# Kernel optimization log

Measured on AMD Instinct MI355X. Metric: run time of the kernel, lower is better.

## Reference

```python
import jax, jax.numpy as jnp
import numpy as np

HUGE = jnp.float32(1e31)   # ops.HUGE_INT
EPS = 1e-20
B, AN = 1024, 256
D = 256            # emb_dim
HD = 512           # history_dim
AD = 2 * D         # action_dim
NE, NR = 100000, 400


def setup_inputs() -> dict:
    key = jax.random.key(0)
    ks = jax.random.split(key, 12)
    e = jax.random.randint(ks[0], (B,), 0, NE)
    q = jax.random.randint(ks[1], (B,), 0, NR)
    hstate = jax.random.normal(ks[2], (B, HD), dtype=jnp.float32)
    r_space = jax.random.randint(ks[3], (B, AN), 0, NR)
    e_space = jax.random.randint(ks[4], (B, AN), 0, NE)
    # binary action mask; guarantee at least one valid action per row
    action_mask = (jax.random.uniform(ks[5], (B, AN)) > 0.2).astype(jnp.float32)
    action_mask = action_mask.at[:, 0].set(1.0)
    entity_emb = jax.random.normal(ks[6], (NE, D), dtype=jnp.float32) * 0.02
    relation_emb = jax.random.normal(ks[7], (NR, D), dtype=jnp.float32) * 0.02
    W1 = jax.random.normal(ks[8], (2 * D + HD, AD), dtype=jnp.float32) * (1.0 / np.sqrt(2 * D + HD))
    b1 = jnp.zeros((AD,), dtype=jnp.float32)
    W2 = jax.random.normal(ks[9], (AD, AD), dtype=jnp.float32) * (1.0 / np.sqrt(AD))
    b2 = jnp.zeros((AD,), dtype=jnp.float32)
    return {"e": e, "q": q, "hstate": hstate, "r_space": r_space,
            "e_space": e_space, "action_mask": action_mask,
            "entity_emb": entity_emb, "relation_emb": relation_emb,
            "W1": W1, "b1": b1, "W2": W2, "b2": b2}


def reference(e, q, hstate, r_space, e_space, action_mask,
              entity_emb, relation_emb, W1, b1, W2, b2):
    Q = relation_emb[q]                       # [B, D]
    E = entity_emb[e]                         # [B, D]
    X = jnp.concatenate([E, hstate, Q], axis=-1)          # [B, 2D+HD]
    X = jax.nn.relu(X @ W1 + b1)                          # [B, AD]
    X2 = X @ W2 + b2                                      # [B, AD]
    # action embeddings: [rel_emb[r]; ent_emb[e]] per padded action slot
    A = jnp.concatenate([relation_emb[r_space], entity_emb[e_space]], axis=-1)  # [B, AN, AD]
    scores = jnp.einsum('bad,bd->ba', A, X2) - (1.0 - action_mask) * HUGE      # [B, AN]
    action_dist = jax.nn.softmax(scores, axis=-1)
    entropy = -jnp.sum(action_dist * jnp.log(jnp.clip(action_dist, EPS)), axis=-1)  # [B]
    return action_dist, entropy
```

## Files before the change

### kernel.cpp

```cpp
#include <hip/hip_runtime.h>
#include <math.h>

#define NB   1024
#define NACT 256
#define DIM  256
#define HDIM 512
#define ADIM 512
#define KTOT 1024
#define NE   100000
#define NR   400
#define NRP  448

typedef __attribute__((ext_vector_type(8))) short bf16x8;
typedef __attribute__((ext_vector_type(4))) float f32x4;

__device__ __forceinline__ unsigned short f2bf(float f) {
    unsigned int u = __float_as_uint(f);
    u += 0x7FFF + ((u >> 16) & 1);
    return (unsigned short)(u >> 16);
}
__device__ __forceinline__ float bf2f(unsigned short u) {
    return __uint_as_float(((unsigned int)u) << 16);
}
__device__ __forceinline__ ushort4 cvt4(float4 v) {
    ushort4 o = {f2bf(v.x), f2bf(v.y), f2bf(v.z), f2bf(v.w)};
    return o;
}

__global__ __launch_bounds__(256) void prep_transpose(
    const float* __restrict__ W1, const float* __restrict__ W2,
    const float* __restrict__ rel,
    ushort* __restrict__ W1T, ushort* __restrict__ W2T,
    ushort* __restrict__ relbf)
{
    const int z = blockIdx.z;
    const int tid = threadIdx.x;
    if (z == 2) {
        const int flat = blockIdx.x * 8 + blockIdx.y;
        const int j = flat * 200 + tid;
        if (tid < 200)
            ((ushort4*)relbf)[j] = cvt4(((const float4*)rel)[j]);
        return;
    }
    __shared__ float t[64][68];
    if (z && blockIdx.x >= 8) return;
    const int Kd = z ? 512 : 1024;
    const float* in = z ? W2 : W1;
    ushort* out = z ? W2T : W1T;
    const int k0 = blockIdx.x * 64, n0 = blockIdx.y * 64;
    const int kr = tid >> 2, c = tid & 3;
    #pragma unroll
    for (int j = 0; j < 4; ++j) {
        const float4 v = *(const float4*)(in + (size_t)(k0 + kr) * ADIM + n0 + c * 16 + j * 4);
        *(float4*)&t[kr][c * 16 + j * 4] = v;
    }
    __syncthreads();
    const int nr = tid >> 2;
    ushort tmp[16];
    #pragma unroll
    for (int kk = 0; kk < 16; ++kk) tmp[kk] = f2bf(t[c * 16 + kk][nr]);
    *(uint4*)(out + (size_t)(n0 + nr) * Kd + k0 + c * 16)     = *(uint4*)&tmp[0];
    *(uint4*)(out + (size_t)(n0 + nr) * Kd + k0 + c * 16 + 8) = *(uint4*)&tmp[8];
}

__global__ __launch_bounds__(256) void gemm1_mfma(
    const float* __restrict__ ent, const float* __restrict__ rel,
    const float* __restrict__ hstate,
    const int* __restrict__ e, const int* __restrict__ q,
    const ushort* __restrict__ W1T, const float* __restrict__ b1,
    ushort* __restrict__ Hbf)
{
    const int tid = threadIdx.x;
    __shared__ __align__(16) ushort Als[64][40];
    __shared__ __align__(16) ushort Bls[64][40];

    const int g  = blockIdx.x;
    const int n0 = (g & 7) * 64;
    const int m0 = (g >> 3) * 64;
    const int wave = tid >> 6, lane = tid & 63;
    const int qq   = lane >> 4, l15 = lane & 15;
    const int sm   = tid >> 2, sc = tid & 3;
    const int kofs = sc * 8;

    const int row   = m0 + sm;
    const float* rowE = ent + (size_t)e[row] * DIM;
    const float* rowH = hstate + (size_t)row * HDIM - DIM;
    const float* rowQ = rel + (size_t)q[row] * DIM - (DIM + HDIM);
    const uint4* gb = (const uint4*)(W1T + (size_t)(n0 + sm) * KTOT) + sc;

    f32x4 acc[4];
    #pragma unroll
    for (int mt = 0; mt < 4; ++mt) acc[mt] = (f32x4){0.f, 0.f, 0.f, 0.f};

    float4 pa0 = *(const float4*)(rowE + kofs);
    float4 pa1 = *(const float4*)(rowE + kofs + 4);
    uint4  pb  = gb[0];

    for (int it = 0; it < KTOT / 32; ++it) {
        ushort t8[8];
        t8[0] = f2bf(pa0.x); t8[1] = f2bf(pa0.y); t8[2] = f2bf(pa0.z); t8[3] = f2bf(pa0.w);
        t8[4] = f2bf(pa1.x); t8[5] = f2bf(pa1.y); t8[6] = f2bf(pa1.z); t8[7] = f2bf(pa1.w);
        *(uint4*)&Als[sm][sc * 8] = *(uint4*)t8;
        *(uint4*)&Bls[sm][sc * 8] = pb;
        __syncthreads();
        if (it + 1 < KTOT / 32) {
            const int kg = (it + 1) * 32 + kofs;
            const float* src = (kg < DIM) ? rowE : ((kg < DIM + HDIM) ? rowH : rowQ);
            pa0 = *(const float4*)(src + kg);
            pa1 = *(const float4*)(src + kg + 4);
            pb  = gb[(it + 1) * 4];
        }
        const bf16x8 bfrag = *(const bf16x8*)&Bls[wave * 16 + l15][qq * 8];
        #pragma unroll
        for (int mt = 0; mt < 4; ++mt) {
            const bf16x8 afrag = *(const bf16x8*)&Als[mt * 16 + l15][qq * 8];
            acc[mt] = __builtin_amdgcn_mfma_f32_16x16x32_bf16(afrag, bfrag, acc[mt], 0, 0, 0);
        }
        __syncthreads();
    }
    const int n = n0 + wave * 16 + l15;
    const float bv = b1[n];
    #pragma unroll
    for (int mt = 0; mt < 4; ++mt)
        #pragma unroll
        for (int r = 0; r < 4; ++r) {
            const int m = m0 + mt * 16 + qq * 4 + r;
            Hbf[(size_t)m * ADIM + n] = f2bf(fmaxf(acc[mt][r] + bv, 0.0f));
        }
}

__global__ __launch_bounds__(256) void gemm2_mfma(
    const ushort* __restrict__ A, const ushort* __restrict__ Bt,
    const float* __restrict__ bias, float* __restrict__ X2up,
    ushort* __restrict__ X2rbf)
{
    __shared__ __align__(16) ushort Als[64][40];
    __shared__ __align__(16) ushort Bls[64][40];
    const int tid  = threadIdx.x;
    const int n0   = blockIdx.x * 64;
    const int m0   = blockIdx.y * 64;
    const int wave = tid >> 6, lane = tid & 63;
    const int qq   = lane >> 4, l15 = lane & 15;
    const int sm   = tid >> 2, sc = tid & 3;

    const uint4* ga = (const uint4*)(A  + (size_t)(m0 + sm) * ADIM) + sc;
    const uint4* gb = (const uint4*)(Bt + (size_t)(n0 + sm) * ADIM) + sc;

    f32x4 acc[4];
    #pragma unroll
    for (int mt = 0; mt < 4; ++mt) acc[mt] = (f32x4){0.f, 0.f, 0.f, 0.f};

    uint4 pa = ga[0], pb = gb[0];
    for (int it = 0; it < ADIM / 32; ++it) {
        *(uint4*)&Als[sm][sc * 8] = pa;
        *(uint4*)&Bls[sm][sc * 8] = pb;
        __syncthreads();
        if (it + 1 < ADIM / 32) {
            pa = ga[(it + 1) * 4];
            pb = gb[(it + 1) * 4];
        }
        const bf16x8 bfrag = *(const bf16x8*)&Bls[wave * 16 + l15][qq * 8];
        #pragma unroll
        for (int mt = 0; mt < 4; ++mt) {
            const bf16x8 afrag = *(const bf16x8*)&Als[mt * 16 + l15][qq * 8];
            acc[mt] = __builtin_amdgcn_mfma_f32_16x16x32_bf16(afrag, bfrag, acc[mt], 0, 0, 0);
        }
        __syncthreads();
    }
    const int n = n0 + wave * 16 + l15;
    const float bv = bias[n];
    #pragma unroll
    for (int mt = 0; mt < 4; ++mt)
        #pragma unroll
        for (int r = 0; r < 4; ++r) {
            const int m = m0 + mt * 16 + qq * 4 + r;
            const float v = acc[mt][r] + bv;
            if (n < 256) X2rbf[(size_t)m * DIM + n] = f2bf(v);
            else         X2up [(size_t)m * DIM + (n - 256)] = v;
        }
}

__global__ __launch_bounds__(256) void gemm_rel(
    const ushort* __restrict__ A, const ushort* __restrict__ Bt,
    float* __restrict__ R)
{
    __shared__ __align__(16) ushort Als[64][40];
    __shared__ __align__(16) ushort Bls[64][40];
    const int tid  = threadIdx.x;
    const int n0   = blockIdx.x * 64;
    const int m0   = blockIdx.y * 64;
    const int wave = tid >> 6, lane = tid & 63;
    const int qq   = lane >> 4, l15 = lane & 15;
    const int sm   = tid >> 2, sc = tid & 3;

    const int brow = (n0 + sm < NR) ? (n0 + sm) : (NR - 1);
    const uint4* ga = (const uint4*)(A  + (size_t)(m0 + sm) * DIM) + sc;
    const uint4* gb = (const uint4*)(Bt + (size_t)brow * DIM) + sc;

    f32x4 acc[4];
    #pragma unroll
    for (int mt = 0; mt < 4; ++mt) acc[mt] = (f32x4){0.f, 0.f, 0.f, 0.f};

    uint4 pa = ga[0], pb = gb[0];
    for (int it = 0; it < DIM / 32; ++it) {
        *(uint4*)&Als[sm][sc * 8] = pa;
        *(uint4*)&Bls[sm][sc * 8] = pb;
        __syncthreads();
        if (it + 1 < DIM / 32) {
            pa = ga[(it + 1) * 4];
            pb = gb[(it + 1) * 4];
        }
        const bf16x8 bfrag = *(const bf16x8*)&Bls[wave * 16 + l15][qq * 8];
        #pragma unroll
        for (int mt = 0; mt < 4; ++mt) {
            const bf16x8 afrag = *(const bf16x8*)&Als[mt * 16 + l15][qq * 8];
            acc[mt] = __builtin_amdgcn_mfma_f32_16x16x32_bf16(afrag, bfrag, acc[mt], 0, 0, 0);
        }
        __syncthreads();
    }
    const int n = n0 + wave * 16 + l15;
    if (n < NR) {
        #pragma unroll
        for (int mt = 0; mt < 4; ++mt)
            #pragma unroll
            for (int r = 0; r < 4; ++r) {
                const int m = m0 + mt * 16 + qq * 4 + r;
                R[(size_t)m * NRP + n] = acc[mt][r];
            }
    }
}

__global__ __launch_bounds__(512) void scores_kernel(
    const int* __restrict__ r_space, const int* __restrict__ e_space,
    const float* __restrict__ amask,
    const float* __restrict__ ent, const float* __restrict__ R,
    const float* __restrict__ X2up,
    float* __restrict__ dist_out, float* __restrict__ ent_out)
{
    const int b    = blockIdx.x;
    const int tid  = threadIdx.x;
    const int wave = tid >> 6;
    const int lane = tid & 63;

    __shared__ float xs[DIM];
    __shared__ float sc[NACT];
    __shared__ int   ridx[NACT];
    __shared__ int   eidx[NACT];
    __shared__ float red1[8], red2[8], red3[8];

    if (tid < NACT) ridx[tid] = r_space[(size_t)b * NACT + tid];
    else            eidx[tid - NACT] = e_space[(size_t)b * NACT + tid - NACT];
    if (tid < DIM / 4)
        ((float4*)xs)[tid] = ((const float4*)(X2up + (size_t)b * DIM))[tid];
    __syncthreads();

    const float4 xe = ((const float4*)xs)[lane];
    const float* R_row = R + (size_t)b * NRP;

    const int abase = wave * 32;
    for (int a0 = abase; a0 < abase + 32; a0 += 16) {
        const float rsc = (lane < 16) ? R_row[ridx[a0 + lane]] : 0.0f;
        float4 ev[16];
        #pragma unroll
        for (int i = 0; i < 16; ++i)
            ev[i] = ((const float4*)(ent + (size_t)eidx[a0 + i] * DIM))[lane];
        float p[16];
        #pragma unroll
        for (int i = 0; i < 16; ++i)
            p[i] = ev[i].x * xe.x + ev[i].y * xe.y + ev[i].z * xe.z + ev[i].w * xe.w;
        #pragma unroll
        for (int off = 32; off; off >>= 1) {
            #pragma unroll
            for (int i = 0; i < 16; ++i) p[i] += __shfl_xor(p[i], off);
        }
        float out = p[0];
        #pragma unroll
        for (int i = 1; i < 16; ++i) out = (lane == i) ? p[i] : out;
        if (lane < 16) sc[a0 + lane] = out + rsc;
    }
    __syncthreads();

    float s = -3.0e38f;
    if (tid < NACT) {
        const float m = amask[(size_t)b * NACT + tid];
        s = sc[tid] - (1.0f - m) * 1e31f;
    }

    float mx = s;
    #pragma unroll
    for (int off = 32; off; off >>= 1) mx = fmaxf(mx, __shfl_xor(mx, off));
    if (lane == 0) red1[wave] = mx;
    __syncthreads();
    mx = red1[0];
    #pragma unroll
    for (int w = 1; w < 8; ++w) mx = fmaxf(mx, red1[w]);

    const float ex = (tid < NACT) ? expf(s - mx) : 0.0f;
    float sum = ex;
    #pragma unroll
    for (int off = 32; off; off >>= 1) sum += __shfl_xor(sum, off);
    if (lane == 0) red2[wave] = sum;
    __syncthreads();
    sum = ((red2[0] + red2[1]) + (red2[2] + red2[3]))
        + ((red2[4] + red2[5]) + (red2[6] + red2[7]));

    const float d = ex / sum;
    if (tid < NACT) dist_out[(size_t)b * NACT + tid] = d;

    float t = (tid < NACT) ? d * logf(fmaxf(d, 1e-20f)) : 0.0f;
    #pragma unroll
    for (int off = 32; off; off >>= 1) t += __shfl_xor(t, off);
    if (lane == 0) red3[wave] = t;
    __syncthreads();
    if (tid == 0)
        ent_out[b] = -(((red3[0] + red3[1]) + (red3[2] + red3[3]))
                     + ((red3[4] + red3[5]) + (red3[6] + red3[7])));
}

extern "C" void kernel_launch(void* const* d_in, const int* in_sizes, int n_in,
                              void* d_out, int out_size, void* d_ws, size_t ws_size,
                              hipStream_t stream) {
    const int*   e       = (const int*)d_in[0];
    const int*   q       = (const int*)d_in[1];
    const float* hstate  = (const float*)d_in[2];
    const int*   r_space = (const int*)d_in[3];
    const int*   e_space = (const int*)d_in[4];
    const float* amask   = (const float*)d_in[5];
    const float* ent     = (const float*)d_in[6];
    const float* rel     = (const float*)d_in[7];
    const float* W1      = (const float*)d_in[8];
    const float* b1      = (const float*)d_in[9];
    const float* W2      = (const float*)d_in[10];
    const float* b2      = (const float*)d_in[11];

    ushort* W1T   = (ushort*)d_ws;
    ushort* W2T   = W1T   + (size_t)ADIM * KTOT;
    ushort* Hbf   = W2T   + (size_t)ADIM * ADIM;
    ushort* relbf = Hbf   + (size_t)NB * ADIM;
    ushort* X2rbf = relbf + (size_t)NR * DIM;
    float*  X2up  = (float*)(X2rbf + (size_t)NB * DIM);
    float*  Rtab  = X2up + (size_t)NB * DIM;
    float*  dist  = (float*)d_out;
    float*  entr  = dist + (size_t)NB * NACT;

    prep_transpose<<<dim3(16, 8, 3), 256, 0, stream>>>(W1, W2, rel, W1T, W2T, relbf);
    gemm1_mfma<<<128, 256, 0, stream>>>(ent, rel, hstate, e, q, W1T, b1, Hbf);
    gemm2_mfma<<<dim3(ADIM / 64, NB / 64), 256, 0, stream>>>(Hbf, W2T, b2, X2up, X2rbf);
    gemm_rel<<<dim3(NRP / 64, NB / 64), 256, 0, stream>>>(X2rbf, relbf, Rtab);
    scores_kernel<<<NB, 512, 0, stream>>>(
        r_space, e_space, amask, ent, Rtab, X2up, dist, entr);
}
```

Before: 228.1 us.

## Fold relation GEMM into W2 via precomputed rel·W2 and split-K GEMMs

Precomputes rel_emb·W2_low (a 400x512 product) so the relation score table comes straight out of the second GEMM, which removes the separate gemm_rel launch and the bf16 X2 round trip. GEMM1 is split-K into four partial buffers to get more blocks, and the reduction, bias and ReLU are fused into the second GEMM's A-operand load. The second GEMM is also split-K by two, so the scores kernel has to add the two partials. In exchange there is more fp32 partial traffic and a different bf16 rounding path for the relation scores.

```diff
diff --git a/kernel.cpp b/kernel.cpp
--- a/kernel.cpp
+++ b/kernel.cpp
@@ -10,6 +10,7 @@
 #define NE   100000
 #define NR   400
 #define NRP  448
+#define NCAT 704
 
 typedef __attribute__((ext_vector_type(8))) short bf16x8;
 typedef __attribute__((ext_vector_type(4))) float f32x4;
@@ -19,95 +20,147 @@
     u += 0x7FFF + ((u >> 16) & 1);
     return (unsigned short)(u >> 16);
 }
-__device__ __forceinline__ float bf2f(unsigned short u) {
-    return __uint_as_float(((unsigned int)u) << 16);
-}
 __device__ __forceinline__ ushort4 cvt4(float4 v) {
     ushort4 o = {f2bf(v.x), f2bf(v.y), f2bf(v.z), f2bf(v.w)};
     return o;
 }
 
-__global__ __launch_bounds__(256) void prep_transpose(
+__global__ __launch_bounds__(256) void prep_kernel(
     const float* __restrict__ W1, const float* __restrict__ W2,
-    const float* __restrict__ rel,
-    ushort* __restrict__ W1T, ushort* __restrict__ W2T,
-    ushort* __restrict__ relbf)
+    const float* __restrict__ rel, const float* __restrict__ b2,
+    ushort* __restrict__ W1T, ushort* __restrict__ Bcat,
+    ushort* __restrict__ W2lowbf, ushort* __restrict__ relbf,
+    float* __restrict__ cvec)
 {
-    const int z = blockIdx.z;
-    const int tid = threadIdx.x;
-    if (z == 2) {
-        const int flat = blockIdx.x * 8 + blockIdx.y;
-        const int j = flat * 200 + tid;
-        if (tid < 200)
-            ((ushort4*)relbf)[j] = cvt4(((const float4*)rel)[j]);
-        return;
-    }
-    __shared__ float t[64][68];
-    if (z && blockIdx.x >= 8) return;
-    const int Kd = z ? 512 : 1024;
-    const float* in = z ? W2 : W1;
-    ushort* out = z ? W2T : W1T;
-    const int k0 = blockIdx.x * 64, n0 = blockIdx.y * 64;
-    const int kr = tid >> 2, c = tid & 3;
-    #pragma unroll
-    for (int j = 0; j < 4; ++j) {
-        const float4 v = *(const float4*)(in + (size_t)(k0 + kr) * ADIM + n0 + c * 16 + j * 4);
-        *(float4*)&t[kr][c * 16 + j * 4] = v;
-    }
-    __syncthreads();
-    const int nr = tid >> 2;
-    ushort tmp[16];
-    #pragma unroll
-    for (int kk = 0; kk < 16; ++kk) tmp[kk] = f2bf(t[c * 16 + kk][nr]);
-    *(uint4*)(out + (size_t)(n0 + nr) * Kd + k0 + c * 16)     = *(uint4*)&tmp[0];
-    *(uint4*)(out + (size_t)(n0 + nr) * Kd + k0 + c * 16 + 8) = *(uint4*)&tmp[8];
-}
-
-__global__ __launch_bounds__(256) void gemm1_mfma(
+    const int blk = blockIdx.x, tid = threadIdx.x;
+    if (blk < 160) {
+        __shared__ float t[64][68];
+        const float* in; ushort* out; int Kd, k0, n0, rowbase;
+        if (blk < 128) {
+            in = W1; out = W1T; Kd = 1024;
+            k0 = (blk >> 3) * 64; n0 = (blk & 7) * 64; rowbase = n0;
+        } else {
+            const int l = blk - 128;
+            in = W2; out = Bcat; Kd = 512;
+            k0 = (l >> 2) * 64; n0 = 256 + (l & 3) * 64; rowbase = n0 - 256;
+        }
+        const int kr = tid >> 2, c = tid & 3;
+        #pragma unroll
+        for (int j = 0; j < 4; ++j) {
+            const float4 v = *(const float4*)(in + (size_t)(k0 + kr) * ADIM + n0 + c * 16 + j * 4);
+            *(float4*)&t[kr][c * 16 + j * 4] = v;
+        }
+        __syncthreads();
+        const int nr = tid >> 2;
+        ushort tmp[16];
+        #pragma unroll
+        for (int kk = 0; kk < 16; ++kk) tmp[kk] = f2bf(t[c * 16 + kk][nr]);
+        *(uint4*)(out + (size_t)(rowbase + nr) * Kd + k0 + c * 16)     = *(uint4*)&tmp[0];
+        *(uint4*)(out + (size_t)(rowbase + nr) * Kd + k0 + c * 16 + 8) = *(uint4*)&tmp[8];
+    } else if (blk < 288) {
+        const int l = blk - 160;
+        const int row = l * 4 + (tid >> 6);
+        const int d4  = tid & 63;
+        const float4 v = *(const float4*)(W2 + (size_t)row * ADIM + d4 * 4);
+        *(ushort4*)(W2lowbf + (size_t)row * DIM + d4 * 4) = cvt4(v);
+    } else if (blk < 388) {
+        const int j = (blk - 288) * 256 + tid;
+        ((ushort4*)relbf)[j] = cvt4(((const float4*)rel)[j]);
+    } else {
+        const int r = (blk - 388) * 256 + tid;
+        if (r < NRP) {
+            const int rr = (r < NR) ? r : (NR - 1);
+            const float* a = rel + (size_t)rr * DIM;
+            float s = 0.f;
+            for (int d = 0; d < DIM; d += 4) {
+                const float4 av = *(const float4*)(a + d);
+                const float4 bv = *(const float4*)(b2 + d);
+                s += av.x * bv.x + av.y * bv.y + av.z * bv.z + av.w * bv.w;
+            }
+            cvec[r] = s;
+        }
+    }
+}
+
+__global__ __launch_bounds__(256) void mega2_kernel(
     const float* __restrict__ ent, const float* __restrict__ rel,
     const float* __restrict__ hstate,
     const int* __restrict__ e, const int* __restrict__ q,
-    const ushort* __restrict__ W1T, const float* __restrict__ b1,
-    ushort* __restrict__ Hbf)
+    const ushort* __restrict__ W1T, const ushort* __restrict__ relbf,
+    const ushort* __restrict__ W2lowbf,
+    ushort* __restrict__ Bcat, float* __restrict__ Hpart)
 {
-    const int tid = threadIdx.x;
     __shared__ __align__(16) ushort Als[64][40];
     __shared__ __align__(16) ushort Bls[64][40];
-
-    const int g  = blockIdx.x;
-    const int n0 = (g & 7) * 64;
-    const int m0 = (g >> 3) * 64;
+    const int blk = blockIdx.x, tid = threadIdx.x;
     const int wave = tid >> 6, lane = tid & 63;
     const int qq   = lane >> 4, l15 = lane & 15;
     const int sm   = tid >> 2, sc = tid & 3;
-    const int kofs = sc * 8;
-
-    const int row   = m0 + sm;
-    const float* rowE = ent + (size_t)e[row] * DIM;
-    const float* rowH = hstate + (size_t)row * HDIM - DIM;
-    const float* rowQ = rel + (size_t)q[row] * DIM - (DIM + HDIM);
-    const uint4* gb = (const uint4*)(W1T + (size_t)(n0 + sm) * KTOT) + sc;
 
     f32x4 acc[4];
     #pragma unroll
     for (int mt = 0; mt < 4; ++mt) acc[mt] = (f32x4){0.f, 0.f, 0.f, 0.f};
 
-    float4 pa0 = *(const float4*)(rowE + kofs);
-    float4 pa1 = *(const float4*)(rowE + kofs + 4);
+    if (blk < 56) {
+        const int n0 = (blk & 7) * 64;
+        const int m0 = (blk >> 3) * 64;
+        const int arow = (m0 + sm < NR) ? (m0 + sm) : (NR - 1);
+        const uint4* ga = (const uint4*)(relbf + (size_t)arow * DIM) + sc;
+        const uint4* gb = (const uint4*)(W2lowbf + (size_t)(n0 + sm) * DIM) + sc;
+        uint4 pa = ga[0], pb = gb[0];
+        for (int it = 0; it < DIM / 32; ++it) {
+            *(uint4*)&Als[sm][sc * 8] = pa;
+            *(uint4*)&Bls[sm][sc * 8] = pb;
+            __syncthreads();
+            if (it + 1 < DIM / 32) { pa = ga[(it + 1) * 4]; pb = gb[(it + 1) * 4]; }
+            const bf16x8 bfrag = *(const bf16x8*)&Bls[wave * 16 + l15][qq * 8];
+            #pragma unroll
+            for (int mt = 0; mt < 4; ++mt) {
+                const bf16x8 afrag = *(const bf16x8*)&Als[mt * 16 + l15][qq * 8];
+                acc[mt] = __builtin_amdgcn_mfma_f32_16x16x32_bf16(afrag, bfrag, acc[mt], 0, 0, 0);
+            }
+            __syncthreads();
+        }
+        const int n = n0 + wave * 16 + l15;
+        #pragma unroll
+        for (int mt = 0; mt < 4; ++mt)
+            #pragma unroll
+            for (int r = 0; r < 4; ++r) {
+                const int m = m0 + mt * 16 + qq * 4 + r;
+                Bcat[(size_t)(256 + m) * ADIM + n] = f2bf(acc[mt][r]);
+            }
+        return;
+    }
+
+    const int g  = blk - 56;
+    const int n0 = (g & 7) * 64;
+    const int m0 = ((g >> 3) & 15) * 64;
+    const int z  = g >> 7;
+    const int kbase = z * 256;
+    const int kofs  = sc * 8;
+
+    const int row = m0 + sm;
+    const float* abase;
+    if (z == 0)      abase = ent + (size_t)e[row] * DIM;
+    else if (z == 3) abase = rel + (size_t)q[row] * DIM;
+    else             abase = hstate + (size_t)row * HDIM + (kbase - DIM);
+    const uint4* gb = (const uint4*)(W1T + (size_t)(n0 + sm) * KTOT + kbase) + sc;
+
+    float4 pa0 = *(const float4*)(abase + kofs);
+    float4 pa1 = *(const float4*)(abase + kofs + 4);
     uint4  pb  = gb[0];
 
-    for (int it = 0; it < KTOT / 32; ++it) {
+    for (int it = 0; it < 8; ++it) {
         ushort t8[8];
         t8[0] = f2bf(pa0.x); t8[1] = f2bf(pa0.y); t8[2] = f2bf(pa0.z); t8[3] = f2bf(pa0.w);
         t8[4] = f2bf(pa1.x); t8[5] = f2bf(pa1.y); t8[6] = f2bf(pa1.z); t8[7] = f2bf(pa1.w);
         *(uint4*)&Als[sm][sc * 8] = *(uint4*)t8;
         *(uint4*)&Bls[sm][sc * 8] = pb;
         __syncthreads();
-        if (it + 1 < KTOT / 32) {
-            const int kg = (it + 1) * 32 + kofs;
-            const float* src = (kg < DIM) ? rowE : ((kg < DIM + HDIM) ? rowH : rowQ);
-            pa0 = *(const float4*)(src + kg);
-            pa1 = *(const float4*)(src + kg + 4);
+        if (it + 1 < 8) {
+            const int lofs = (it + 1) * 32 + kofs;
+            pa0 = *(const float4*)(abase + lofs);
+            pa1 = *(const float4*)(abase + lofs + 4);
             pb  = gb[(it + 1) * 4];
         }
         const bf16x8 bfrag = *(const bf16x8*)&Bls[wave * 16 + l15][qq * 8];
@@ -118,46 +171,82 @@
         }
         __syncthreads();
     }
+    float* dst = Hpart + (size_t)z * NB * ADIM;
     const int n = n0 + wave * 16 + l15;
-    const float bv = b1[n];
     #pragma unroll
     for (int mt = 0; mt < 4; ++mt)
         #pragma unroll
         for (int r = 0; r < 4; ++r) {
             const int m = m0 + mt * 16 + qq * 4 + r;
-            Hbf[(size_t)m * ADIM + n] = f2bf(fmaxf(acc[mt][r] + bv, 0.0f));
-        }
-}
-
-__global__ __launch_bounds__(256) void gemm2_mfma(
-    const ushort* __restrict__ A, const ushort* __restrict__ Bt,
-    const float* __restrict__ bias, float* __restrict__ X2up,
-    ushort* __restrict__ X2rbf)
+            dst[(size_t)m * ADIM + n] = acc[mt][r];
+        }
+}
+
+__global__ __launch_bounds__(256) void gemm2big(
+    const float* __restrict__ Hpart, const float* __restrict__ b1,
+    const ushort* __restrict__ Bcat, const float* __restrict__ b2,
+    const float* __restrict__ cvec,
+    float* __restrict__ X2upPart, float* __restrict__ RtabPart)
 {
     __shared__ __align__(16) ushort Als[64][40];
     __shared__ __align__(16) ushort Bls[64][40];
     const int tid  = threadIdx.x;
     const int n0   = blockIdx.x * 64;
     const int m0   = blockIdx.y * 64;
+    const int z    = blockIdx.z;
+    const int kb   = z * 256;
     const int wave = tid >> 6, lane = tid & 63;
     const int qq   = lane >> 4, l15 = lane & 15;
     const int sm   = tid >> 2, sc = tid & 3;
 
-    const uint4* ga = (const uint4*)(A  + (size_t)(m0 + sm) * ADIM) + sc;
-    const uint4* gb = (const uint4*)(Bt + (size_t)(n0 + sm) * ADIM) + sc;
+    const size_t arow = (size_t)(m0 + sm) * ADIM + kb;
+    const uint4* gbp = (const uint4*)(Bcat + (size_t)(n0 + sm) * ADIM + kb) + sc;
 
     f32x4 acc[4];
     #pragma unroll
     for (int mt = 0; mt < 4; ++mt) acc[mt] = (f32x4){0.f, 0.f, 0.f, 0.f};
 
-    uint4 pa = ga[0], pb = gb[0];
-    for (int it = 0; it < ADIM / 32; ++it) {
-        *(uint4*)&Als[sm][sc * 8] = pa;
-        *(uint4*)&Bls[sm][sc * 8] = pb;
+    float4 pz[4][2], pb1[2];
+    uint4  pbv;
+    {
+        const int lk = sc * 8;
+        pb1[0] = *(const float4*)(b1 + kb + lk);
+        pb1[1] = *(const float4*)(b1 + kb + lk + 4);
+        #pragma unroll
+        for (int z4 = 0; z4 < 4; ++z4) {
+            const float* hp = Hpart + (size_t)z4 * NB * ADIM + arow + lk;
+            pz[z4][0] = *(const float4*)hp;
+            pz[z4][1] = *(const float4*)(hp + 4);
+        }
+        pbv = gbp[0];
+    }
+
+    for (int it = 0; it < 8; ++it) {
+        float4 s0 = pb1[0], s1 = pb1[1];
+        #pragma unroll
+        for (int z4 = 0; z4 < 4; ++z4) {
+            s0.x += pz[z4][0].x; s0.y += pz[z4][0].y; s0.z += pz[z4][0].z; s0.w += pz[z4][0].w;
+            s1.x += pz[z4][1].x; s1.y += pz[z4][1].y; s1.z += pz[z4][1].z; s1.w += pz[z4][1].w;
+        }
+        ushort t8[8];
+        t8[0] = f2bf(fmaxf(s0.x, 0.f)); t8[1] = f2bf(fmaxf(s0.y, 0.f));
+        t8[2] = f2bf(fmaxf(s0.z, 0.f)); t8[3] = f2bf(fmaxf(s0.w, 0.f));
+        t8[4] = f2bf(fmaxf(s1.x, 0.f)); t8[5] = f2bf(fmaxf(s1.y, 0.f));
+        t8[6] = f2bf(fmaxf(s1.z, 0.f)); t8[7] = f2bf(fmaxf(s1.w, 0.f));
+        *(uint4*)&Als[sm][sc * 8] = *(uint4*)t8;
+        *(uint4*)&Bls[sm][sc * 8] = pbv;
         __syncthreads();
-        if (it + 1 < ADIM / 32) {
-            pa = ga[(it + 1) * 4];
-            pb = gb[(it + 1) * 4];
+        if (it + 1 < 8) {
+            const int lk = (it + 1) * 32 + sc * 8;
+            pb1[0] = *(const float4*)(b1 + kb + lk);
+            pb1[1] = *(const float4*)(b1 + kb + lk + 4);
+            #pragma unroll
+            for (int z4 = 0; z4 < 4; ++z4) {
+                const float* hp = Hpart + (size_t)z4 * NB * ADIM + arow + lk;
+                pz[z4][0] = *(const float4*)hp;
+                pz[z4][1] = *(const float4*)(hp + 4);
+            }
+            pbv = gbp[(it + 1) * 4];
         }
         const bf16x8 bfrag = *(const bf16x8*)&Bls[wave * 16 + l15][qq * 8];
         #pragma unroll
@@ -168,73 +257,23 @@
         __syncthreads();
     }
     const int n = n0 + wave * 16 + l15;
-    const float bv = bias[n];
+    const float extra = (z == 0) ? ((n < 256) ? b2[256 + n] : cvec[n - 256]) : 0.0f;
     #pragma unroll
     for (int mt = 0; mt < 4; ++mt)
         #pragma unroll
         for (int r = 0; r < 4; ++r) {
             const int m = m0 + mt * 16 + qq * 4 + r;
-            const float v = acc[mt][r] + bv;
-            if (n < 256) X2rbf[(size_t)m * DIM + n] = f2bf(v);
-            else         X2up [(size_t)m * DIM + (n - 256)] = v;
-        }
-}
-
-__global__ __launch_bounds__(256) void gemm_rel(
-    const ushort* __restrict__ A, const ushort* __restrict__ Bt,
-    float* __restrict__ R)
-{
-    __shared__ __align__(16) ushort Als[64][40];
-    __shared__ __align__(16) ushort Bls[64][40];
-    const int tid  = threadIdx.x;
-    const int n0   = blockIdx.x * 64;
-    const int m0   = blockIdx.y * 64;
-    const int wave = tid >> 6, lane = tid & 63;
-    const int qq   = lane >> 4, l15 = lane & 15;
-    const int sm   = tid >> 2, sc = tid & 3;
-
-    const int brow = (n0 + sm < NR) ? (n0 + sm) : (NR - 1);
-    const uint4* ga = (const uint4*)(A  + (size_t)(m0 + sm) * DIM) + sc;
-    const uint4* gb = (const uint4*)(Bt + (size_t)brow * DIM) + sc;
-
-    f32x4 acc[4];
-    #pragma unroll
-    for (int mt = 0; mt < 4; ++mt) acc[mt] = (f32x4){0.f, 0.f, 0.f, 0.f};
-
-    uint4 pa = ga[0], pb = gb[0];
-    for (int it = 0; it < DIM / 32; ++it) {
-        *(uint4*)&Als[sm][sc * 8] = pa;
-        *(uint4*)&Bls[sm][sc * 8] = pb;
-        __syncthreads();
-        if (it + 1 < DIM / 32) {
-            pa = ga[(it + 1) * 4];
-            pb = gb[(it + 1) * 4];
-        }
-        const bf16x8 bfrag = *(const bf16x8*)&Bls[wave * 16 + l15][qq * 8];
-        #pragma unroll
-        for (int mt = 0; mt < 4; ++mt) {
-            const bf16x8 afrag = *(const bf16x8*)&Als[mt * 16 + l15][qq * 8];
-            acc[mt] = __builtin_amdgcn_mfma_f32_16x16x32_bf16(afrag, bfrag, acc[mt], 0, 0, 0);
-        }
-        __syncthreads();
-    }
-    const int n = n0 + wave * 16 + l15;
-    if (n < NR) {
-        #pragma unroll
-        for (int mt = 0; mt < 4; ++mt)
-            #pragma unroll
-            for (int r = 0; r < 4; ++r) {
-                const int m = m0 + mt * 16 + qq * 4 + r;
-                R[(size_t)m * NRP + n] = acc[mt][r];
-            }
-    }
+            const float v = acc[mt][r] + extra;
+            if (n < 256) X2upPart[(size_t)z * NB * DIM + (size_t)m * DIM + n] = v;
+            else         RtabPart[(size_t)z * NB * NRP + (size_t)m * NRP + (n - 256)] = v;
+        }
 }
 
 __global__ __launch_bounds__(512) void scores_kernel(
     const int* __restrict__ r_space, const int* __restrict__ e_space,
     const float* __restrict__ amask,
-    const float* __restrict__ ent, const float* __restrict__ R,
-    const float* __restrict__ X2up,
+    const float* __restrict__ ent,
+    const float* __restrict__ RtabPart, const float* __restrict__ X2upPart,
     float* __restrict__ dist_out, float* __restrict__ ent_out)
 {
     const int b    = blockIdx.x;
@@ -250,16 +289,25 @@
 
     if (tid < NACT) ridx[tid] = r_space[(size_t)b * NACT + tid];
     else            eidx[tid - NACT] = e_space[(size_t)b * NACT + tid - NACT];
-    if (tid < DIM / 4)
-        ((float4*)xs)[tid] = ((const float4*)(X2up + (size_t)b * DIM))[tid];
+    if (tid < DIM / 4) {
+        float4 v0 = ((const float4*)(X2upPart + (size_t)b * DIM))[tid];
+        const float4 v1 = ((const float4*)(X2upPart + (size_t)NB * DIM + (size_t)b * DIM))[tid];
+        v0.x += v1.x; v0.y += v1.y; v0.z += v1.z; v0.w += v1.w;
+        ((float4*)xs)[tid] = v0;
+    }
     __syncthreads();
 
     const float4 xe = ((const float4*)xs)[lane];
-    const float* R_row = R + (size_t)b * NRP;
+    const float* R0 = RtabPart + (size_t)b * NRP;
+    const float* R1 = RtabPart + (size_t)NB * NRP + (size_t)b * NRP;
 
     const int abase = wave * 32;
     for (int a0 = abase; a0 < abase + 32; a0 += 16) {
-        const float rsc = (lane < 16) ? R_row[ridx[a0 + lane]] : 0.0f;
+        float rsc = 0.0f;
+        if (lane < 16) {
+            const int ri = ridx[a0 + lane];
+            rsc = R0[ri] + R1[ri];
+        }
         float4 ev[16];
         #pragma unroll
         for (int i = 0; i < 16; ++i)
@@ -333,20 +381,20 @@
     const float* W2      = (const float*)d_in[10];
     const float* b2      = (const float*)d_in[11];
 
-    ushort* W1T   = (ushort*)d_ws;
-    ushort* W2T   = W1T   + (size_t)ADIM * KTOT;
-    ushort* Hbf   = W2T   + (size_t)ADIM * ADIM;
-    ushort* relbf = Hbf   + (size_t)NB * ADIM;
-    ushort* X2rbf = relbf + (size_t)NR * DIM;
-    float*  X2up  = (float*)(X2rbf + (size_t)NB * DIM);
-    float*  Rtab  = X2up + (size_t)NB * DIM;
-    float*  dist  = (float*)d_out;
-    float*  entr  = dist + (size_t)NB * NACT;
-
-    prep_transpose<<<dim3(16, 8, 3), 256, 0, stream>>>(W1, W2, rel, W1T, W2T, relbf);
-    gemm1_mfma<<<128, 256, 0, stream>>>(ent, rel, hstate, e, q, W1T, b1, Hbf);
-    gemm2_mfma<<<dim3(ADIM / 64, NB / 64), 256, 0, stream>>>(Hbf, W2T, b2, X2up, X2rbf);
-    gemm_rel<<<dim3(NRP / 64, NB / 64), 256, 0, stream>>>(X2rbf, relbf, Rtab);
+    ushort* W1T    = (ushort*)d_ws;
+    ushort* Bcat   = W1T    + (size_t)ADIM * KTOT;
+    ushort* W2low  = Bcat   + (size_t)NCAT * ADIM;
+    ushort* relbf  = W2low  + (size_t)ADIM * DIM;
+    float*  cvec   = (float*)(relbf + (size_t)NR * DIM);
+    float*  Hpart  = cvec   + NRP;
+    float*  X2upP  = Hpart  + (size_t)4 * NB * ADIM;
+    float*  RtabP  = X2upP  + (size_t)2 * NB * DIM;
+    float*  dist   = (float*)d_out;
+    float*  entr   = dist + (size_t)NB * NACT;
+
+    prep_kernel<<<390, 256, 0, stream>>>(W1, W2, rel, b2, W1T, Bcat, W2low, relbf, cvec);
+    mega2_kernel<<<568, 256, 0, stream>>>(ent, rel, hstate, e, q, W1T, relbf, W2low, Bcat, Hpart);
+    gemm2big<<<dim3(11, 16, 2), 256, 0, stream>>>(Hpart, b1, Bcat, b2, cvec, X2upP, RtabP);
     scores_kernel<<<NB, 512, 0, stream>>>(
-        r_space, e_space, amask, ent, Rtab, X2up, dist, entr);
-}
+        r_space, e_space, amask, ent, RtabP, X2upP, dist, entr);
+}
```

New measurement: 223.0 us. 2.2% less time.
